# Optimization experiments

Measured on AMD Instinct MI355X. Metric: run time of the kernel, lower is better.

Reference implementation:

```python
import jax, jax.numpy as jnp
import numpy as np

NUM_HEADS = 8
EPS = 1e-12  # torch F.normalize eps


def _l2norm(t):
    n = jnp.linalg.norm(t, axis=-1, keepdims=True)
    return t / jnp.maximum(n, EPS)


def setup_inputs() -> dict:
    key = jax.random.key(0)
    ks = jax.random.split(key, 8)
    b, hw, c = 1, 4096, 64
    scale = 1.0 / np.sqrt(c)
    return {
        "x": jax.random.normal(ks[0], (b, hw, c), jnp.float32),
        "y": jax.random.normal(ks[1], (b, hw, c), jnp.float32),
        "Wq": jax.random.normal(ks[2], (c, c), jnp.float32) * scale,
        "bq": jax.random.normal(ks[3], (c,), jnp.float32) * 0.02,
        "Wkv": jax.random.normal(ks[4], (c, 2 * c), jnp.float32) * scale,
        "bkv": jax.random.normal(ks[5], (2 * c,), jnp.float32) * 0.02,
        "We": jax.random.normal(ks[6], (c, c), jnp.float32) * scale,
        "be": jax.random.normal(ks[7], (c,), jnp.float32) * 0.02,
    }


def reference(x, y, Wq, bq, Wkv, bkv, We, be):
    b, hw, c = x.shape
    H = NUM_HEADS
    d = c // H

    # q projection -> [b, H, hw, d]
    q = (x @ Wq + bq).reshape(b, hw, H, d).transpose(0, 2, 1, 3)
    # kv projection -> k, v each [b, H, hw, d]
    kv = (y @ Wkv + bkv).reshape(b, hw, 2, H, d)
    k = kv[:, :, 0].transpose(0, 2, 1, 3)
    v = kv[:, :, 1].transpose(0, 2, 1, 3)

    # cosine-normalized attention (no 1/sqrt(d) scale in original)
    q = _l2norm(q)
    k = _l2norm(k)
    attn = jnp.einsum("bhqd,bhkd->bhqk", q, k)  # [b, H, hw, hw]
    attn = jax.nn.softmax(attn, axis=-1)
    out = jnp.einsum("bhqk,bhkd->bhqd", attn, v)  # [b, H, hw, d]

    # merge heads -> [b, hw, c], then output projection
    out = out.transpose(0, 2, 1, 3).reshape(b, hw, c)
    return out @ We + be
```

## Files before the change

kernel.cpp:

```cpp
#include <hip/hip_runtime.h>

#define HW 4096
#define C 64
#define H 8
#define D 8
#define S 8
#define KEYS_PER_SPLIT (HW / S)
#define TILES (KEYS_PER_SPLIT / 16)
#define L2E 1.44269504088896340736f
#define VROW 1032

typedef _Float16 h2 __attribute__((ext_vector_type(2)));
typedef _Float16 half4 __attribute__((ext_vector_type(4)));
typedef float f32x4 __attribute__((ext_vector_type(4)));

static __device__ __forceinline__ float fast_exp2(float x) {
#if __has_builtin(__builtin_amdgcn_exp2f)
    return __builtin_amdgcn_exp2f(x);
#else
    return __exp2f(x);
#endif
}

static __device__ __forceinline__ h2 pack_h2(float a, float b) {
    return __builtin_bit_cast(h2, __builtin_amdgcn_cvt_pkrtz(a, b));
}

static __device__ __forceinline__ half4 cat_h2(h2 lo, h2 hi) {
    uint2 u;
    u.x = __builtin_bit_cast(unsigned, lo);
    u.y = __builtin_bit_cast(unsigned, hi);
    return __builtin_bit_cast(half4, u);
}

static __device__ __forceinline__ f32x4 mfma16(half4 a, half4 b, f32x4 c) {
    return __builtin_amdgcn_mfma_f32_16x16x16f16(a, b, c, 0, 0, 0);
}

static __device__ __forceinline__ float gnorm8(float a) {
    float ss = a * a;
    ss += __shfl_xor(ss, 1, 64);
    ss += __shfl_xor(ss, 2, 64);
    ss += __shfl_xor(ss, 4, 64);
    return 1.0f / fmaxf(sqrtf(ss), 1e-12f);
}

__global__ __launch_bounds__(192) void proj_kernel(
    const float* __restrict__ x, const float* __restrict__ y,
    const float* __restrict__ Wq, const float* __restrict__ bq,
    const float* __restrict__ Wkv, const float* __restrict__ bkv,
    _Float16* __restrict__ qh, _Float16* __restrict__ kh, _Float16* __restrict__ vt)
{
    const int r0 = blockIdx.x * 4;
    const int wave = __builtin_amdgcn_readfirstlane((int)(threadIdx.x >> 6));
    const int j = threadIdx.x & 63;

    const float* __restrict__ W;
    const float* __restrict__ rows;
    int wstride;
    float bias;
    if (wave == 0)      { W = Wq + j;        wstride = C;     bias = bq[j];      rows = x + (size_t)r0 * C; }
    else if (wave == 1) { W = Wkv + j;       wstride = 2 * C; bias = bkv[j];     rows = y + (size_t)r0 * C; }
    else                { W = Wkv + C + j;   wstride = 2 * C; bias = bkv[C + j]; rows = y + (size_t)r0 * C; }

    float a0 = bias, a1 = bias, a2 = bias, a3 = bias;
    #pragma unroll
    for (int i = 0; i < C; ++i) {
        const float w = W[(size_t)i * wstride];
        a0 = fmaf(rows[i],         w, a0);
        a1 = fmaf(rows[C + i],     w, a1);
        a2 = fmaf(rows[2 * C + i], w, a2);
        a3 = fmaf(rows[3 * C + i], w, a3);
    }

    const int head = j >> 3;
    const int d = j & 7;
    if (wave == 0) {
        const float s0 = gnorm8(a0) * L2E, s1 = gnorm8(a1) * L2E;
        const float s2 = gnorm8(a2) * L2E, s3 = gnorm8(a3) * L2E;
        _Float16* p = qh + ((size_t)head * HW + r0) * D + d;
        p[0 * D] = (_Float16)(a0 * s0);
        p[1 * D] = (_Float16)(a1 * s1);
        p[2 * D] = (_Float16)(a2 * s2);
        p[3 * D] = (_Float16)(a3 * s3);
    } else if (wave == 1) {
        const float s0 = gnorm8(a0), s1 = gnorm8(a1);
        const float s2 = gnorm8(a2), s3 = gnorm8(a3);
        _Float16* p = kh + ((size_t)head * HW + r0) * D + d;
        p[0 * D] = (_Float16)(a0 * s0);
        p[1 * D] = (_Float16)(a1 * s1);
        p[2 * D] = (_Float16)(a2 * s2);
        p[3 * D] = (_Float16)(a3 * s3);
    } else {
        const h2 lo = pack_h2(a0, a1);
        const h2 hi = pack_h2(a2, a3);
        uint2 u;
        u.x = __builtin_bit_cast(unsigned, lo);
        u.y = __builtin_bit_cast(unsigned, hi);
        *(half4*)(vt + (size_t)j * HW + r0) = __builtin_bit_cast(half4, u);
    }
}

__global__ __launch_bounds__(512, 8) void attn_kernel(
    const _Float16* __restrict__ qh, const _Float16* __restrict__ kh,
    const _Float16* __restrict__ vt, float* __restrict__ po, float* __restrict__ pl)
{
    __shared__ __align__(16) char smem[512 * 16 + 16 * VROW];
    char* sV = smem + 512 * 16;

    const int tid = threadIdx.x;
    const int wave = __builtin_amdgcn_readfirstlane(tid >> 6);
    const int lane = tid & 63;
    const int n = lane & 15;
    const int quad = lane >> 4;

    const int b = blockIdx.x;
    const int h = b & 7;
    const int qg = (b >> 3) & 15;
    const int split = b >> 7;
    const int q0 = qg * 256 + wave * 32;
    const int k0 = split * KEYS_PER_SPLIT;

    const _Float16* __restrict__ qhh = qh + (size_t)h * HW * D;
    const _Float16* __restrict__ khh = kh + (size_t)h * HW * D;
    const _Float16* __restrict__ vth = vt + (size_t)h * D * HW;

    {
        const uint4 kd = *(const uint4*)(khh + (size_t)(k0 + tid) * D);
        *(uint4*)(smem + tid * 16) = kd;
    }
    {
        const uint4 vd = *(const uint4*)(vth + (size_t)wave * HW + k0 + lane * 8);
        char* dst = sV + wave * VROW + lane * 16;
        *(uint2*)dst       = make_uint2(vd.x, vd.y);
        *(uint2*)(dst + 8) = make_uint2(vd.z, vd.w);
    }
    if (tid < 256) *(unsigned*)(sV + 8 * VROW + tid * 4) = 0x3C003C00u;

    const half4 z4 = {};
    half4 qf0 = z4, qf1 = z4;
    if (quad < 2) {
        qf0 = *(const half4*)(qhh + (size_t)(q0 + n) * D + quad * 4);
        qf1 = *(const half4*)(qhh + (size_t)(q0 + 16 + n) * D + quad * 4);
    }

    __syncthreads();

    f32x4 o0 = {}, o1 = {};
    const int kOff = n * 16 + (quad & 1) * 8;
    const int vOff = n * VROW + quad * 8;

    #pragma unroll 8
    for (int t = 0; t < TILES; ++t) {
        const half4 kf = __builtin_bit_cast(half4, *(const uint2*)(smem + kOff + t * 256));
        const half4 vf = __builtin_bit_cast(half4, *(const uint2*)(sV + vOff + t * 32));
        const f32x4 zc = {};
        f32x4 c0 = mfma16(kf, qf0, zc);
        f32x4 c1 = mfma16(kf, qf1, zc);
        const h2 lo0 = pack_h2(fast_exp2(c0[0]), fast_exp2(c0[1]));
        const h2 hi0 = pack_h2(fast_exp2(c0[2]), fast_exp2(c0[3]));
        const h2 lo1 = pack_h2(fast_exp2(c1[0]), fast_exp2(c1[1]));
        const h2 hi1 = pack_h2(fast_exp2(c1[2]), fast_exp2(c1[3]));
        o0 = mfma16(vf, cat_h2(lo0, hi0), o0);
        o1 = mfma16(vf, cat_h2(lo1, hi1), o1);
    }

    const size_t pbase = (size_t)(split * H + h) * HW;
    if (quad < 2) {
        *(float4*)(po + (pbase + q0 + n) * 8 + quad * 4)      = make_float4(o0[0], o0[1], o0[2], o0[3]);
        *(float4*)(po + (pbase + q0 + 16 + n) * 8 + quad * 4) = make_float4(o1[0], o1[1], o1[2], o1[3]);
    } else if (quad == 2) {
        pl[pbase + q0 + n]      = o0[0];
        pl[pbase + q0 + 16 + n] = o1[0];
    }
}

__global__ __launch_bounds__(256) void outproj_kernel(
    const float* __restrict__ po, const float* __restrict__ pl,
    const float* __restrict__ We, const float* __restrict__ be,
    float* __restrict__ out)
{
    const int t = threadIdx.x;
    const int wave = __builtin_amdgcn_readfirstlane((int)(t >> 6));
    const int lane = t & 63;
    const int rbase = blockIdx.x * 16 + wave * 4;
    const int head = lane >> 3;
    const int d = lane & 7;

    __shared__ float sO[16][64];

    #pragma unroll
    for (int rr = 0; rr < 4; ++rr) {
        const int r = rbase + rr;
        float os = 0.f, ls = 0.f;
        #pragma unroll
        for (int s = 0; s < S; ++s) {
            os += po[((size_t)(s * H + head) * HW + r) * 8 + d];
            ls += pl[(size_t)(s * H + head) * HW + r];
        }
        sO[wave * 4 + rr][lane] = os / ls;
    }
    __syncthreads();

    const float bias = be[lane];
    float a0 = bias, a1 = bias, a2 = bias, a3 = bias;
    #pragma unroll
    for (int i4 = 0; i4 < 16; ++i4) {
        const int i = i4 * 4;
        const float4 o0 = *(const float4*)&sO[wave * 4 + 0][i];
        const float4 o1 = *(const float4*)&sO[wave * 4 + 1][i];
        const float4 o2 = *(const float4*)&sO[wave * 4 + 2][i];
        const float4 o3 = *(const float4*)&sO[wave * 4 + 3][i];
        const float w0 = We[(size_t)(i + 0) * C + lane];
        const float w1 = We[(size_t)(i + 1) * C + lane];
        const float w2 = We[(size_t)(i + 2) * C + lane];
        const float w3 = We[(size_t)(i + 3) * C + lane];
        a0 = fmaf(o0.x, w0, a0); a0 = fmaf(o0.y, w1, a0); a0 = fmaf(o0.z, w2, a0); a0 = fmaf(o0.w, w3, a0);
        a1 = fmaf(o1.x, w0, a1); a1 = fmaf(o1.y, w1, a1); a1 = fmaf(o1.z, w2, a1); a1 = fmaf(o1.w, w3, a1);
        a2 = fmaf(o2.x, w0, a2); a2 = fmaf(o2.y, w1, a2); a2 = fmaf(o2.z, w2, a2); a2 = fmaf(o2.w, w3, a2);
        a3 = fmaf(o3.x, w0, a3); a3 = fmaf(o3.y, w1, a3); a3 = fmaf(o3.z, w2, a3); a3 = fmaf(o3.w, w3, a3);
    }
    out[(size_t)(rbase + 0) * C + lane] = a0;
    out[(size_t)(rbase + 1) * C + lane] = a1;
    out[(size_t)(rbase + 2) * C + lane] = a2;
    out[(size_t)(rbase + 3) * C + lane] = a3;
}

extern "C" void kernel_launch(void* const* d_in, const int* in_sizes, int n_in,
                              void* d_out, int out_size, void* d_ws, size_t ws_size,
                              hipStream_t stream) {
    const float* x   = (const float*)d_in[0];
    const float* y   = (const float*)d_in[1];
    const float* Wq  = (const float*)d_in[2];
    const float* bq  = (const float*)d_in[3];
    const float* Wkv = (const float*)d_in[4];
    const float* bkv = (const float*)d_in[5];
    const float* We  = (const float*)d_in[6];
    const float* be  = (const float*)d_in[7];
    float* out = (float*)d_out;

    char* ws = (char*)d_ws;
    _Float16* qh = (_Float16*)(ws);
    _Float16* kh = (_Float16*)(ws + (512u << 10));
    _Float16* vt = (_Float16*)(ws + (1024u << 10));
    float*    po = (float*)   (ws + (1536u << 10));
    float*    pl = (float*)   (ws + (10240u << 10));

    hipLaunchKernelGGL(proj_kernel, dim3(HW / 4), dim3(192), 0, stream,
                       x, y, Wq, bq, Wkv, bkv, qh, kh, vt);
    hipLaunchKernelGGL(attn_kernel, dim3(H * (HW / 256) * S), dim3(512), 0, stream,
                       qh, kh, vt, po, pl);
    hipLaunchKernelGGL(outproj_kernel, dim3(HW / 16), dim3(256), 0, stream,
                       po, pl, We, be, out);
}
```

Baseline: 97.86 us.

## Switch attention inner loop to 32x32x8 MFMA tiles

```diff
diff --git a/kernel.cpp b/kernel.cpp
--- a/kernel.cpp
+++ b/kernel.cpp
@@ -6,13 +6,15 @@
 #define D 8
 #define S 8
 #define KEYS_PER_SPLIT (HW / S)
-#define TILES (KEYS_PER_SPLIT / 16)
+#define TILES (KEYS_PER_SPLIT / 32)
 #define L2E 1.44269504088896340736f
+#define KROW 24
 #define VROW 1032
 
 typedef _Float16 h2 __attribute__((ext_vector_type(2)));
 typedef _Float16 half4 __attribute__((ext_vector_type(4)));
 typedef float f32x4 __attribute__((ext_vector_type(4)));
+typedef float f32x16 __attribute__((ext_vector_type(16)));
 
 static __device__ __forceinline__ float fast_exp2(float x) {
 #if __has_builtin(__builtin_amdgcn_exp2f)
@@ -33,8 +35,8 @@
     return __builtin_bit_cast(half4, u);
 }
 
-static __device__ __forceinline__ f32x4 mfma16(half4 a, half4 b, f32x4 c) {
-    return __builtin_amdgcn_mfma_f32_16x16x16f16(a, b, c, 0, 0, 0);
+static __device__ __forceinline__ f32x16 mfma32(half4 a, half4 b, f32x16 c) {
+    return __builtin_amdgcn_mfma_f32_32x32x8f16(a, b, c, 0, 0, 0);
 }
 
 static __device__ __forceinline__ float gnorm8(float a) {
@@ -94,10 +96,7 @@
     } else {
         const h2 lo = pack_h2(a0, a1);
         const h2 hi = pack_h2(a2, a3);
-        uint2 u;
-        u.x = __builtin_bit_cast(unsigned, lo);
-        u.y = __builtin_bit_cast(unsigned, hi);
-        *(half4*)(vt + (size_t)j * HW + r0) = __builtin_bit_cast(half4, u);
+        *(half4*)(vt + (size_t)j * HW + r0) = cat_h2(lo, hi);
     }
 }
 
@@ -105,14 +104,14 @@
     const _Float16* __restrict__ qh, const _Float16* __restrict__ kh,
     const _Float16* __restrict__ vt, float* __restrict__ po, float* __restrict__ pl)
 {
-    __shared__ __align__(16) char smem[512 * 16 + 16 * VROW];
-    char* sV = smem + 512 * 16;
+    __shared__ __align__(16) char smem[512 * KROW + 16 * VROW];
+    char* sV = smem + 512 * KROW;
 
     const int tid = threadIdx.x;
     const int wave = __builtin_amdgcn_readfirstlane(tid >> 6);
     const int lane = tid & 63;
-    const int n = lane & 15;
-    const int quad = lane >> 4;
+    const int m = lane & 31;
+    const int half = lane >> 5;
 
     const int b = blockIdx.x;
     const int h = b & 7;
@@ -127,7 +126,9 @@
 
     {
         const uint4 kd = *(const uint4*)(khh + (size_t)(k0 + tid) * D);
-        *(uint4*)(smem + tid * 16) = kd;
+        char* dst = smem + tid * KROW;
+        *(uint2*)dst       = make_uint2(kd.x, kd.y);
+        *(uint2*)(dst + 8) = make_uint2(kd.z, kd.w);
     }
     {
         const uint4 vd = *(const uint4*)(vth + (size_t)wave * HW + k0 + lane * 8);
@@ -137,42 +138,36 @@
     }
     if (tid < 256) *(unsigned*)(sV + 8 * VROW + tid * 4) = 0x3C003C00u;
 
-    const half4 z4 = {};
-    half4 qf0 = z4, qf1 = z4;
-    if (quad < 2) {
-        qf0 = *(const half4*)(qhh + (size_t)(q0 + n) * D + quad * 4);
-        qf1 = *(const half4*)(qhh + (size_t)(q0 + 16 + n) * D + quad * 4);
-    }
+    const half4 qf = __builtin_bit_cast(half4,
+        *(const uint2*)(qhh + (size_t)(q0 + m) * D + half * 4));
 
     __syncthreads();
 
-    f32x4 o0 = {}, o1 = {};
-    const int kOff = n * 16 + (quad & 1) * 8;
-    const int vOff = n * VROW + quad * 8;
-
-    #pragma unroll 8
+    f32x16 O = {};
+    const int kBase = m * KROW + half * 8;
+    const int vBase = (lane & 15) * VROW + half * 8;
+
+    #pragma unroll 4
     for (int t = 0; t < TILES; ++t) {
-        const half4 kf = __builtin_bit_cast(half4, *(const uint2*)(smem + kOff + t * 256));
-        const half4 vf = __builtin_bit_cast(half4, *(const uint2*)(sV + vOff + t * 32));
-        const f32x4 zc = {};
-        f32x4 c0 = mfma16(kf, qf0, zc);
-        f32x4 c1 = mfma16(kf, qf1, zc);
-        const h2 lo0 = pack_h2(fast_exp2(c0[0]), fast_exp2(c0[1]));
-        const h2 hi0 = pack_h2(fast_exp2(c0[2]), fast_exp2(c0[3]));
-        const h2 lo1 = pack_h2(fast_exp2(c1[0]), fast_exp2(c1[1]));
-        const h2 hi1 = pack_h2(fast_exp2(c1[2]), fast_exp2(c1[3]));
-        o0 = mfma16(vf, cat_h2(lo0, hi0), o0);
-        o1 = mfma16(vf, cat_h2(lo1, hi1), o1);
+        const half4 kf = __builtin_bit_cast(half4,
+            *(const uint2*)(smem + kBase + t * (32 * KROW)));
+        const f32x16 zc = {};
+        const f32x16 c = mfma32(kf, qf, zc);
+
+        #pragma unroll
+        for (int j = 0; j < 4; ++j) {
+            const h2 lo = pack_h2(fast_exp2(c[4 * j + 0]), fast_exp2(c[4 * j + 1]));
+            const h2 hi = pack_h2(fast_exp2(c[4 * j + 2]), fast_exp2(c[4 * j + 3]));
+            const half4 pb = cat_h2(lo, hi);
+            const half4 vf = __builtin_bit_cast(half4,
+                *(const uint2*)(sV + vBase + t * 64 + j * 16));
+            O = mfma32(vf, pb, O);
+        }
     }
 
     const size_t pbase = (size_t)(split * H + h) * HW;
-    if (quad < 2) {
-        *(float4*)(po + (pbase + q0 + n) * 8 + quad * 4)      = make_float4(o0[0], o0[1], o0[2], o0[3]);
-        *(float4*)(po + (pbase + q0 + 16 + n) * 8 + quad * 4) = make_float4(o1[0], o1[1], o1[2], o1[3]);
-    } else if (quad == 2) {
-        pl[pbase + q0 + n]      = o0[0];
-        pl[pbase + q0 + 16 + n] = o1[0];
-    }
+    *(float4*)(po + (pbase + q0 + m) * 8 + half * 4) = make_float4(O[0], O[1], O[2], O[3]);
+    if (half == 0) pl[pbase + q0 + m] = O[4];
 }
 
 __global__ __launch_bounds__(256) void outproj_kernel(
```

Result: faster. 95.39 us (-2.5%).
